# Kernel optimization log

Hardware: AMD Instinct MI355X
Metric: run time of the kernel (lower is better)

## Reference

```python
import jax, jax.numpy as jnp
import numpy as np

BIG = 1e9
EPS_BETA = 1e-6
EPS_BN = 1e-5

N_NODES = 50000
N_EDGES = 800000
IN_DIM = 128
OUT_DIM = 128


def setup_inputs() -> dict:
    key = jax.random.key(0)
    ks = jax.random.split(key, 8)
    h = jax.random.normal(ks[0], (N_NODES, IN_DIM), dtype=jnp.float32)
    src = jax.random.randint(ks[1], (N_EDGES,), 0, N_NODES, dtype=jnp.int32)
    dst = jax.random.randint(ks[2], (N_EDGES,), 0, N_NODES, dtype=jnp.int32)
    sigma_GD = jax.random.uniform(ks[3], (N_EDGES,), dtype=jnp.float32)
    fc_w = jax.random.normal(ks[4], (IN_DIM, OUT_DIM), dtype=jnp.float32) / np.sqrt(IN_DIM)
    fc_b = jax.random.normal(ks[5], (OUT_DIM,), dtype=jnp.float32) * 0.01
    attn_w = jax.random.normal(ks[6], (2 * OUT_DIM, 1), dtype=jnp.float32) / np.sqrt(2 * OUT_DIM)
    attn_b = jax.random.normal(ks[7], (1,), dtype=jnp.float32) * 0.01
    bn_gamma = jnp.ones((OUT_DIM,), dtype=jnp.float32)
    bn_beta = jnp.zeros((OUT_DIM,), dtype=jnp.float32)
    return {"h": h, "src": src, "dst": dst, "sigma_GD": sigma_GD,
            "fc_w": fc_w, "fc_b": fc_b, "attn_w": attn_w, "attn_b": attn_b,
            "bn_gamma": bn_gamma, "bn_beta": bn_beta}


def reference(h, src, dst, sigma_GD, fc_w, fc_b, attn_w, attn_b, bn_gamma, bn_beta):
    n = h.shape[0]
    # node projection
    z = h @ fc_w + fc_b                                   # [N, D]
    z = jnp.where(jnp.isinf(z), BIG, z)
    # per-edge attention logits: concat(src,dst) @ W == src@W1 + dst@W2 (avoid concat materialization)
    d = z.shape[1]
    w_src, w_dst = attn_w[:d], attn_w[d:]
    z_src = z[src]                                        # [E, D]
    a = z_src @ w_src + z[dst] @ w_dst + attn_b           # [E, 1]
    a = jnp.where(jnp.isinf(a), BIG, a)
    e = jax.nn.leaky_relu(a, negative_slope=0.01)[:, 0]   # [E]
    # segment softmax over incoming edges (mailbox softmax)
    m = jax.ops.segment_max(e, dst, num_segments=n)       # [N]
    ex = jnp.exp(e - m[dst])
    denom = jax.ops.segment_sum(ex, dst, num_segments=n)  # [N]
    alpha = ex / denom[dst]                               # [E]
    # beta: sigma_GD normalized per destination node
    bsum = jax.ops.segment_sum(sigma_GD, dst, num_segments=n)
    beta = sigma_GD / (bsum[dst] + EPS_BETA)              # [E]
    # weighted scatter-sum of source features
    h_new = jax.ops.segment_sum((alpha * beta)[:, None] * z_src, dst, num_segments=n)  # [N, D]
    h_new = jnp.where(jnp.isinf(h_new), BIG, h_new)
    # BatchNorm1d (training-mode batch stats, biased variance, as torch does)
    mu = h_new.mean(axis=0)
    var = ((h_new - mu) ** 2).mean(axis=0)
    h_bn = (h_new - mu) * jax.lax.rsqrt(var + EPS_BN) * bn_gamma + bn_beta
    return jax.nn.elu(h_bn)
```

## Files before the change

### kernel.cpp

```cpp
#include <hip/hip_runtime.h>
#include <hip/hip_fp16.h>
#include <math.h>

#define N_NODES 50000
#define N_EDGES 800000
#define BIGV 1000000000.0f
#define NBLK_GEMM 3125
#define CHUNK 4096
#define NBLK_A 196
#define NBUCKET 196

typedef _Float16 half8 __attribute__((ext_vector_type(8)));
typedef float floatx4 __attribute__((ext_vector_type(4)));

__device__ __forceinline__ float clampinf(float x) { return isinf(x) ? BIGV : x; }

__device__ __forceinline__ void barrier_lgkm_only() {
    __builtin_amdgcn_sched_barrier(0);
    asm volatile("s_waitcnt lgkmcnt(0)" ::: "memory");
    __builtin_amdgcn_s_barrier();
    __builtin_amdgcn_sched_barrier(0);
}

__global__ __launch_bounds__(256) void k_prep(const float* __restrict__ W,
                                              __half* __restrict__ wt,
                                              float* __restrict__ bns,
                                              const int* __restrict__ dst,
                                              int* __restrict__ counts)
{
    __shared__ int hist[NBUCKET];
    const int t = threadIdx.x;
    const int idx = blockIdx.x * 256 + t;
    if (idx < 16384) {
        int n = idx >> 7, k = idx & 127;
        wt[idx] = __float2half(W[k * 128 + n]);
    }
    if (idx < 256) bns[idx] = 0.f;
    if (t < NBUCKET) hist[t] = 0;
    __syncthreads();
    const int base = blockIdx.x * CHUNK;
    for (int i = t; i < CHUNK; i += 256) {
        int e = base + i;
        if (e < N_EDGES) atomicAdd(&hist[dst[e] >> 8], 1);
    }
    __syncthreads();
    if (t < NBUCKET) counts[blockIdx.x * NBUCKET + t] = hist[t];
}

__global__ __launch_bounds__(256) void k_gemm(
    const float* __restrict__ h, const __half* __restrict__ wt,
    const float* __restrict__ bias, const float* __restrict__ attn_w,
    __half* __restrict__ zh, float* __restrict__ sv, float* __restrict__ tv)
{
    __shared__ _Float16 hA[16][136];
    __shared__ float spart[4][16], tpart[4][16];

    const int tid = threadIdx.x;
    const int lane = tid & 63;
    const int wv = tid >> 6;
    const int l16 = lane & 15;
    const int oct = lane >> 4;
    const int n0 = wv << 5;
    const int node0 = blockIdx.x << 4;

    {
        const float4* h4 = (const float4*)(h + (size_t)node0 * 128);
        for (int i = tid; i < 512; i += 256) {
            int r = i >> 5, c4 = i & 31;
            float4 v = h4[i];
            union { __half2 h2[2]; uint2 u; } pk;
            pk.h2[0] = __floats2half2_rn(v.x, v.y);
            pk.h2[1] = __floats2half2_rn(v.z, v.w);
            *(uint2*)&hA[r][c4 << 2] = pk.u;
        }
    }

    half8 bfrag[4][2];
    #pragma unroll
    for (int kk = 0; kk < 4; ++kk)
        #pragma unroll
        for (int t = 0; t < 2; ++t)
            bfrag[kk][t] = *(const half8*)(wt + (size_t)(n0 + t * 16 + l16) * 128
                                              + kk * 32 + oct * 8);

    const float bv0 = bias[n0 + l16],         bv1 = bias[n0 + 16 + l16];
    const float ws0 = attn_w[n0 + l16],       ws1 = attn_w[n0 + 16 + l16];
    const float wd0 = attn_w[128 + n0 + l16], wd1 = attn_w[128 + n0 + 16 + l16];

    barrier_lgkm_only();

    floatx4 acc0 = {0.f, 0.f, 0.f, 0.f};
    floatx4 acc1 = {0.f, 0.f, 0.f, 0.f};
    #pragma unroll
    for (int kk = 0; kk < 4; ++kk) {
        half8 a = *(const half8*)&hA[l16][(kk << 5) + (oct << 3)];
        acc0 = __builtin_amdgcn_mfma_f32_16x16x32_f16(a, bfrag[kk][0], acc0, 0, 0, 0);
        acc1 = __builtin_amdgcn_mfma_f32_16x16x32_f16(a, bfrag[kk][1], acc1, 0, 0, 0);
    }

    float s_acc[4], t_acc[4];
    #pragma unroll
    for (int r = 0; r < 4; ++r) {
        float z0 = clampinf(acc0[r] + bv0);
        float z1 = clampinf(acc1[r] + bv1);
        const int row = (oct << 2) + r;
        zh[(size_t)(node0 + row) * 128 + n0 + l16]      = __float2half(z0);
        zh[(size_t)(node0 + row) * 128 + n0 + 16 + l16] = __float2half(z1);
        s_acc[r] = z0 * ws0 + z1 * ws1;
        t_acc[r] = z0 * wd0 + z1 * wd1;
    }
    #pragma unroll
    for (int r = 0; r < 4; ++r) {
        #pragma unroll
        for (int o = 1; o < 16; o <<= 1) {
            s_acc[r] += __shfl_xor(s_acc[r], o);
            t_acc[r] += __shfl_xor(t_acc[r], o);
        }
    }
    if (l16 == 0) {
        #pragma unroll
        for (int r = 0; r < 4; ++r) {
            spart[wv][(oct << 2) + r] = s_acc[r];
            tpart[wv][(oct << 2) + r] = t_acc[r];
        }
    }
    barrier_lgkm_only();
    if (tid < 16) {
        sv[node0 + tid] = spart[0][tid] + spart[1][tid] + spart[2][tid] + spart[3][tid];
        tv[node0 + tid] = tpart[0][tid] + tpart[1][tid] + tpart[2][tid] + tpart[3][tid];
    }
}

__global__ __launch_bounds__(256) void k_scatterA(const int* __restrict__ dst,
                                                  const int* __restrict__ counts,
                                                  int* __restrict__ tmp,
                                                  int* __restrict__ bbase_g)
{
    __shared__ int cur[NBUCKET];
    __shared__ int stot[256];
    const int t = threadIdx.x;
    const int self = blockIdx.x;
    int pre = 0, tot = 0;
    if (t < NBUCKET) {
        for (int b = 0; b < NBLK_A; ++b) {
            int c = counts[b * NBUCKET + t];
            if (b < self) pre += c;
            tot += c;
        }
    }
    stot[t] = (t < NBUCKET) ? tot : 0;
    __syncthreads();
    for (int off = 1; off < 256; off <<= 1) {
        int u = (t >= off) ? stot[t - off] : 0;
        __syncthreads();
        stot[t] += u;
        __syncthreads();
    }
    if (t < NBUCKET) {
        const int bb = stot[t] - tot;
        cur[t] = bb + pre;
        if (self == 0) bbase_g[t] = bb;
    }
    if (self == 0 && t == 0) bbase_g[NBUCKET] = N_EDGES;
    __syncthreads();
    const int base = self * CHUNK;
    for (int i = t; i < CHUNK; i += 256) {
        int e = base + i;
        if (e < N_EDGES) {
            int pos = atomicAdd(&cur[dst[e] >> 8], 1);
            tmp[pos] = e;
        }
    }
}

__global__ __launch_bounds__(256) void k_binB(
    const int* __restrict__ tmp, const int* __restrict__ bbase_g,
    const int* __restrict__ dst, const int* __restrict__ src,
    const float* __restrict__ sigma,
    const float* __restrict__ sv, const float* __restrict__ tv,
    const float* __restrict__ attn_b,
    int* __restrict__ colptr, float4* __restrict__ recs)
{
    __shared__ int hist[256];
    __shared__ int scn[256];
    __shared__ int cur[256];
    const int t = threadIdx.x;
    const int b = blockIdx.x;
    const int s0 = bbase_g[b];
    const int n = bbase_g[b + 1] - s0;
    hist[t] = 0;
    __syncthreads();
    for (int i = t; i < n; i += 256) {
        int e = tmp[s0 + i];
        atomicAdd(&hist[dst[e] & 255], 1);
    }
    __syncthreads();
    scn[t] = hist[t];
    __syncthreads();
    for (int off = 1; off < 256; off <<= 1) {
        int u = (t >= off) ? scn[t - off] : 0;
        __syncthreads();
        scn[t] += u;
        __syncthreads();
    }
    const int excl = scn[t] - hist[t];
    cur[t] = s0 + excl;
    const int node = (b << 8) + t;
    if (node < N_NODES) colptr[node] = s0 + excl;
    if (b == 0 && t == 0) colptr[N_NODES] = N_EDGES;
    __syncthreads();
    const float ab = attn_b[0];
    for (int i = t; i < n; i += 256) {
        int e = tmp[s0 + i];
        int d = dst[e];
        int pos = atomicAdd(&cur[d & 255], 1);
        int s = src[e];
        float a = sv[s] + tv[d] + ab;
        a = clampinf(a);
        float ev = a > 0.f ? a : 0.01f * a;
        float4 rec;
        rec.x = __int_as_float(s);
        rec.y = sigma[e];
        rec.z = ev;
        rec.w = 0.f;
        recs[pos] = rec;
    }
}

__global__ __launch_bounds__(256) void k_agg(
    const int* __restrict__ colptr, const float4* __restrict__ recs,
    const __half* __restrict__ zh, float* __restrict__ out)
{
    const int lane = threadIdx.x & 63;
    const int node = blockIdx.x * 4 + (threadIdx.x >> 6);
    if (node >= N_NODES) return;
    const int base = colptr[node];
    const int deg = colptr[node + 1] - base;

    const int grp = lane >> 4;
    const int l16 = lane & 15;
    float acc[8] = {0.f, 0.f, 0.f, 0.f, 0.f, 0.f, 0.f, 0.f};

    if (deg > 0) {
        if (deg <= 64) {
            int sidx = 0; float sig = 0.f, e = -INFINITY;
            if (lane < deg) {
                float4 r = recs[base + lane];
                sidx = __float_as_int(r.x); sig = r.y; e = r.z;
            }
            float m = e;
            for (int o = 32; o; o >>= 1) m = fmaxf(m, __shfl_xor(m, o));
            float p = (lane < deg) ? __expf(e - m) : 0.f;
            float dn = p, bs = sig;
            for (int o = 32; o; o >>= 1) {
                dn += __shfl_xor(dn, o);
                bs += __shfl_xor(bs, o);
            }
            const float coef = p * sig * (1.0f / dn) / (bs + 1e-6f);
            for (int c = 0; c < deg; c += 4) {
                const int j = c + grp;
                const int js = (j < deg) ? j : 0;
                float cf = __shfl(coef, js);
                int sj = __shfl(sidx, js);
                if (j < deg) {
                    uint4 raw = *(const uint4*)(zh + ((size_t)sj << 7) + (l16 << 3));
                    const __half2* hp = (const __half2*)&raw;
                    #pragma unroll
                    for (int k = 0; k < 4; ++k) {
                        float2 f = __half22float2(hp[k]);
                        acc[2*k]   = fmaf(cf, f.x, acc[2*k]);
                        acc[2*k+1] = fmaf(cf, f.y, acc[2*k+1]);
                    }
                }
            }
        } else {
            float m = -INFINITY;
            for (int i = lane; i < deg; i += 64) m = fmaxf(m, recs[base + i].z);
            for (int o = 32; o; o >>= 1) m = fmaxf(m, __shfl_xor(m, o));
            float dn = 0.f, bs = 0.f;
            for (int i = lane; i < deg; i += 64) {
                float4 r = recs[base + i];
                dn += __expf(r.z - m); bs += r.y;
            }
            for (int o = 32; o; o >>= 1) {
                dn += __shfl_xor(dn, o);
                bs += __shfl_xor(bs, o);
            }
            const float scale = (1.0f / dn) / (bs + 1e-6f);
            for (int c = 0; c < deg; c += 64) {
                int i = c + lane;
                int sidx = 0; float coef = 0.f;
                if (i < deg) {
                    float4 r = recs[base + i];
                    sidx = __float_as_int(r.x);
                    coef = __expf(r.z - m) * r.y * scale;
                }
                const int cnt2 = min(64, deg - c);
                for (int j = 0; j < cnt2; j += 4) {
                    const int jj = j + grp;
                    const int js = (jj < cnt2) ? jj : 0;
                    float cf = __shfl(coef, js);
                    int sj = __shfl(sidx, js);
                    if (jj < cnt2) {
                        uint4 raw = *(const uint4*)(zh + ((size_t)sj << 7) + (l16 << 3));
                        const __half2* hp = (const __half2*)&raw;
                        #pragma unroll
                        for (int k = 0; k < 4; ++k) {
                            float2 f = __half22float2(hp[k]);
                            acc[2*k]   = fmaf(cf, f.x, acc[2*k]);
                            acc[2*k+1] = fmaf(cf, f.y, acc[2*k+1]);
                        }
                    }
                }
            }
        }
    }
    #pragma unroll
    for (int k = 0; k < 8; ++k) {
        acc[k] += __shfl_xor(acc[k], 16);
        acc[k] += __shfl_xor(acc[k], 32);
    }
    if (grp == 0) {
        float4 o0, o1;
        o0.x = clampinf(acc[0]); o0.y = clampinf(acc[1]);
        o0.z = clampinf(acc[2]); o0.w = clampinf(acc[3]);
        o1.x = clampinf(acc[4]); o1.y = clampinf(acc[5]);
        o1.z = clampinf(acc[6]); o1.w = clampinf(acc[7]);
        float4* op = (float4*)(out + (size_t)node * 128 + (l16 << 3));
        op[0] = o0; op[1] = o1;
    }
}

__global__ __launch_bounds__(256) void k_bnstats(const float* __restrict__ hnew,
                                                 float* __restrict__ sums)
{
    const int tid = threadIdx.x;
    const int f4 = (tid & 31) << 2;
    const int rgrp = tid >> 5;
    float4 s = {0.f, 0.f, 0.f, 0.f}, q = {0.f, 0.f, 0.f, 0.f};
    for (int node = blockIdx.x * 8 + rgrp; node < N_NODES; node += 256 * 8) {
        float4 v = *(const float4*)(hnew + (size_t)node * 128 + f4);
        s.x += v.x; s.y += v.y; s.z += v.z; s.w += v.w;
        q.x += v.x * v.x; q.y += v.y * v.y; q.z += v.z * v.z; q.w += v.w * v.w;
    }
    __shared__ float4 ls[256], lq[256];
    ls[tid] = s; lq[tid] = q;
    __syncthreads();
    for (int off = 128; off >= 32; off >>= 1) {
        if (tid < off) {
            float4 a = ls[tid + off], b = lq[tid + off];
            ls[tid].x += a.x; ls[tid].y += a.y; ls[tid].z += a.z; ls[tid].w += a.w;
            lq[tid].x += b.x; lq[tid].y += b.y; lq[tid].z += b.z; lq[tid].w += b.w;
        }
        __syncthreads();
    }
    if (tid < 32) {
        float4 fs = ls[tid], fq = lq[tid];
        atomicAdd(&sums[f4 + 0], fs.x);
        atomicAdd(&sums[f4 + 1], fs.y);
        atomicAdd(&sums[f4 + 2], fs.z);
        atomicAdd(&sums[f4 + 3], fs.w);
        atomicAdd(&sums[128 + f4 + 0], fq.x);
        atomicAdd(&sums[128 + f4 + 1], fq.y);
        atomicAdd(&sums[128 + f4 + 2], fq.z);
        atomicAdd(&sums[128 + f4 + 3], fq.w);
    }
}

__global__ __launch_bounds__(256) void k_bnapply(float* __restrict__ io,
                                                 const float* __restrict__ sums,
                                                 const float* __restrict__ gamma,
                                                 const float* __restrict__ beta)
{
    __shared__ float sc[128], sh[128];
    const int tid = threadIdx.x;
    if (tid < 128) {
        const float invn = 1.0f / (float)N_NODES;
        float mu = sums[tid] * invn;
        float var = fmaxf(sums[128 + tid] * invn - mu * mu, 0.f);
        float g = gamma[tid] * rsqrtf(var + 1e-5f);
        sc[tid] = g;
        sh[tid] = beta[tid] - mu * g;
    }
    __syncthreads();
    const size_t idx = (size_t)blockIdx.x * 256 + tid;
    const int f4 = ((int)idx & 31) << 2;
    float4 x = ((const float4*)io)[idx];
    float y0 = x.x * sc[f4 + 0] + sh[f4 + 0];
    float y1 = x.y * sc[f4 + 1] + sh[f4 + 1];
    float y2 = x.z * sc[f4 + 2] + sh[f4 + 2];
    float y3 = x.w * sc[f4 + 3] + sh[f4 + 3];
    float4 o;
    o.x = y0 > 0.f ? y0 : expm1f(y0);
    o.y = y1 > 0.f ? y1 : expm1f(y1);
    o.z = y2 > 0.f ? y2 : expm1f(y2);
    o.w = y3 > 0.f ? y3 : expm1f(y3);
    ((float4*)io)[idx] = o;
}

extern "C" void kernel_launch(void* const* d_in, const int* in_sizes, int n_in,
                              void* d_out, int out_size, void* d_ws, size_t ws_size,
                              hipStream_t stream)
{
    const float* h      = (const float*)d_in[0];
    const int*   src    = (const int*)  d_in[1];
    const int*   dst    = (const int*)  d_in[2];
    const float* sigma  = (const float*)d_in[3];
    const float* fc_w   = (const float*)d_in[4];
    const float* fc_b   = (const float*)d_in[5];
    const float* attn_w = (const float*)d_in[6];
    const float* attn_b = (const float*)d_in[7];
    const float* gamma  = (const float*)d_in[8];
    const float* beta   = (const float*)d_in[9];
    float* out = (float*)d_out;

    float4* recs   = (float4*)d_ws;
    __half* zh     = (__half*)(recs + N_EDGES);
    float*  sv     = (float*)(zh + (size_t)N_NODES * 128);
    float*  tv     = sv + N_NODES;
    float*  bns    = tv + N_NODES;
    int*    colptr = (int*)(bns + 256);
    __half* wt     = (__half*)(colptr + 50004);
    int*    counts = (int*)(wt + 128 * 128);
    int*    bbase  = counts + 38416;
    int*    tmp    = bbase + 256;

    k_prep     <<<NBLK_A, 256, 0, stream>>>(fc_w, wt, bns, dst, counts);
    k_scatterA <<<NBLK_A, 256, 0, stream>>>(dst, counts, tmp, bbase);
    k_gemm     <<<NBLK_GEMM, 256, 0, stream>>>(h, wt, fc_b, attn_w, zh, sv, tv);
    k_binB     <<<NBUCKET, 256, 0, stream>>>(tmp, bbase, dst, src, sigma,
                                             sv, tv, attn_b, colptr, recs);
    k_agg      <<<N_NODES / 4, 256, 0, stream>>>(colptr, recs, zh, out);
    k_bnstats  <<<256, 256, 0, stream>>>(out, bns);
    k_bnapply  <<<(N_NODES * 128) / (256 * 4), 256, 0, stream>>>(out, bns, gamma, beta);
}
```

Measured before the change: 251.6 us.

## Move edge record building into bucket scatter and use finer 64-node buckets

The first-pass scatter now computes the attention logit and writes full float4 records, with dst packed in the last slot, into a bucket-sorted temp buffer. The second pass then only re-sorts records within 64-node buckets (782 buckets instead of 196), so there are no indirect re-reads of src/dst/sigma/sv/tv through the edge index. Finer buckets spread the second-pass sort over more blocks and let a wave shuffle replace the 256-entry shared-memory scan. In exchange the temp buffer grows from 4 to 16 bytes per edge, and the scatter kernel has to run after the GEMM, so it can no longer overlap with it.

```diff
diff --git a/kernel.cpp b/kernel.cpp
--- a/kernel.cpp
+++ b/kernel.cpp
@@ -7,8 +7,9 @@
 #define BIGV 1000000000.0f
 #define NBLK_GEMM 3125
 #define CHUNK 4096
-#define NBLK_A 196
-#define NBUCKET 196
+#define NCHUNK 196
+#define NBUCKET 782
+#define NB4 784
 
 typedef _Float16 half8 __attribute__((ext_vector_type(8)));
 typedef float floatx4 __attribute__((ext_vector_type(4)));
@@ -28,7 +29,7 @@
                                               const int* __restrict__ dst,
                                               int* __restrict__ counts)
 {
-    __shared__ int hist[NBUCKET];
+    __shared__ int hist[NB4];
     const int t = threadIdx.x;
     const int idx = blockIdx.x * 256 + t;
     if (idx < 16384) {
@@ -36,15 +37,15 @@
         wt[idx] = __float2half(W[k * 128 + n]);
     }
     if (idx < 256) bns[idx] = 0.f;
-    if (t < NBUCKET) hist[t] = 0;
+    for (int i = t; i < NB4; i += 256) hist[i] = 0;
     __syncthreads();
     const int base = blockIdx.x * CHUNK;
     for (int i = t; i < CHUNK; i += 256) {
         int e = base + i;
-        if (e < N_EDGES) atomicAdd(&hist[dst[e] >> 8], 1);
-    }
-    __syncthreads();
-    if (t < NBUCKET) counts[blockIdx.x * NBUCKET + t] = hist[t];
+        if (e < N_EDGES) atomicAdd(&hist[dst[e] >> 6], 1);
+    }
+    __syncthreads();
+    for (int i = t; i < NB4; i += 256) counts[blockIdx.x * NB4 + i] = hist[i];
 }
 
 __global__ __launch_bounds__(256) void k_gemm(
@@ -131,97 +132,112 @@
     }
 }
 
-__global__ __launch_bounds__(256) void k_scatterA(const int* __restrict__ dst,
-                                                  const int* __restrict__ counts,
-                                                  int* __restrict__ tmp,
-                                                  int* __restrict__ bbase_g)
-{
-    __shared__ int cur[NBUCKET];
-    __shared__ int stot[256];
+__global__ __launch_bounds__(256) void k_scat(
+    const int* __restrict__ src, const int* __restrict__ dst,
+    const float* __restrict__ sigma,
+    const float* __restrict__ sv, const float* __restrict__ tv,
+    const float* __restrict__ attn_b, const int* __restrict__ counts,
+    float4* __restrict__ tmp, int* __restrict__ bbase_g)
+{
+    __shared__ int cur[NB4];
+    __shared__ int tsc[256];
     const int t = threadIdx.x;
     const int self = blockIdx.x;
-    int pre = 0, tot = 0;
-    if (t < NBUCKET) {
-        for (int b = 0; b < NBLK_A; ++b) {
-            int c = counts[b * NBUCKET + t];
-            if (b < self) pre += c;
-            tot += c;
-        }
-    }
-    stot[t] = (t < NBUCKET) ? tot : 0;
+
+    uint4 pre = {0u, 0u, 0u, 0u}, tot = {0u, 0u, 0u, 0u};
+    if (t < 196) {
+        const uint4* c4 = (const uint4*)counts;
+        for (int c = 0; c < NCHUNK; ++c) {
+            uint4 v = c4[c * (NB4 / 4) + t];
+            tot.x += v.x; tot.y += v.y; tot.z += v.z; tot.w += v.w;
+            if (c < self) { pre.x += v.x; pre.y += v.y; pre.z += v.z; pre.w += v.w; }
+        }
+    }
+    const int tsum = (t < 196) ? (int)(tot.x + tot.y + tot.z + tot.w) : 0;
+    tsc[t] = tsum;
     __syncthreads();
     for (int off = 1; off < 256; off <<= 1) {
-        int u = (t >= off) ? stot[t - off] : 0;
+        int u = (t >= off) ? tsc[t - off] : 0;
         __syncthreads();
-        stot[t] += u;
+        tsc[t] += u;
         __syncthreads();
     }
-    if (t < NBUCKET) {
-        const int bb = stot[t] - tot;
-        cur[t] = bb + pre;
-        if (self == 0) bbase_g[t] = bb;
+    if (t < 196) {
+        const int v0 = tsc[t] - tsum;
+        const int v1 = v0 + (int)tot.x;
+        const int v2 = v1 + (int)tot.y;
+        const int v3 = v2 + (int)tot.z;
+        cur[4*t+0] = v0 + (int)pre.x;
+        cur[4*t+1] = v1 + (int)pre.y;
+        cur[4*t+2] = v2 + (int)pre.z;
+        cur[4*t+3] = v3 + (int)pre.w;
+        if (self == 0) {
+            bbase_g[4*t+0] = v0; bbase_g[4*t+1] = v1;
+            bbase_g[4*t+2] = v2; bbase_g[4*t+3] = v3;
+        }
     }
     if (self == 0 && t == 0) bbase_g[NBUCKET] = N_EDGES;
     __syncthreads();
+
+    const float ab = attn_b[0];
     const int base = self * CHUNK;
     for (int i = t; i < CHUNK; i += 256) {
         int e = base + i;
         if (e < N_EDGES) {
-            int pos = atomicAdd(&cur[dst[e] >> 8], 1);
-            tmp[pos] = e;
-        }
-    }
-}
-
-__global__ __launch_bounds__(256) void k_binB(
-    const int* __restrict__ tmp, const int* __restrict__ bbase_g,
-    const int* __restrict__ dst, const int* __restrict__ src,
-    const float* __restrict__ sigma,
-    const float* __restrict__ sv, const float* __restrict__ tv,
-    const float* __restrict__ attn_b,
-    int* __restrict__ colptr, float4* __restrict__ recs)
-{
-    __shared__ int hist[256];
-    __shared__ int scn[256];
-    __shared__ int cur[256];
+            int s = src[e];
+            int d = dst[e];
+            float a = sv[s] + tv[d] + ab;
+            a = clampinf(a);
+            float ev = a > 0.f ? a : 0.01f * a;
+            int pos = atomicAdd(&cur[d >> 6], 1);
+            float4 rec;
+            rec.x = __int_as_float(s);
+            rec.y = sigma[e];
+            rec.z = ev;
+            rec.w = __int_as_float(d);
+            tmp[pos] = rec;
+        }
+    }
+}
+
+__global__ __launch_bounds__(256) void k_binB(const float4* __restrict__ tmp,
+                                              const int* __restrict__ bbase_g,
+                                              int* __restrict__ colptr,
+                                              float4* __restrict__ recs)
+{
+    __shared__ int hist[64];
+    __shared__ int cur[64];
     const int t = threadIdx.x;
     const int b = blockIdx.x;
     const int s0 = bbase_g[b];
     const int n = bbase_g[b + 1] - s0;
-    hist[t] = 0;
-    __syncthreads();
+    if (t < 64) hist[t] = 0;
+    __syncthreads();
+    const float* tw = (const float*)tmp;
     for (int i = t; i < n; i += 256) {
-        int e = tmp[s0 + i];
-        atomicAdd(&hist[dst[e] & 255], 1);
-    }
-    __syncthreads();
-    scn[t] = hist[t];
-    __syncthreads();
-    for (int off = 1; off < 256; off <<= 1) {
-        int u = (t >= off) ? scn[t - off] : 0;
-        __syncthreads();
-        scn[t] += u;
-        __syncthreads();
-    }
-    const int excl = scn[t] - hist[t];
-    cur[t] = s0 + excl;
-    const int node = (b << 8) + t;
-    if (node < N_NODES) colptr[node] = s0 + excl;
+        int d = __float_as_int(tw[4 * (size_t)(s0 + i) + 3]);
+        atomicAdd(&hist[d & 63], 1);
+    }
+    __syncthreads();
+    if (t < 64) {
+        const int hv = hist[t];
+        int x = hv;
+        #pragma unroll
+        for (int o = 1; o < 64; o <<= 1) {
+            int u = __shfl_up(x, o);
+            if (t >= o) x += u;
+        }
+        const int excl = x - hv;
+        cur[t] = s0 + excl;
+        const int node = (b << 6) + t;
+        if (node < N_NODES) colptr[node] = s0 + excl;
+    }
     if (b == 0 && t == 0) colptr[N_NODES] = N_EDGES;
     __syncthreads();
-    const float ab = attn_b[0];
     for (int i = t; i < n; i += 256) {
-        int e = tmp[s0 + i];
-        int d = dst[e];
-        int pos = atomicAdd(&cur[d & 255], 1);
-        int s = src[e];
-        float a = sv[s] + tv[d] + ab;
-        a = clampinf(a);
-        float ev = a > 0.f ? a : 0.01f * a;
-        float4 rec;
-        rec.x = __int_as_float(s);
-        rec.y = sigma[e];
-        rec.z = ev;
+        float4 rec = tmp[s0 + i];
+        int d = __float_as_int(rec.w);
+        int pos = atomicAdd(&cur[d & 63], 1);
         rec.w = 0.f;
         recs[pos] = rec;
     }
@@ -415,22 +431,22 @@
     float* out = (float*)d_out;
 
     float4* recs   = (float4*)d_ws;
-    __half* zh     = (__half*)(recs + N_EDGES);
+    float4* tmp    = recs + N_EDGES;
+    __half* zh     = (__half*)(tmp + N_EDGES);
     float*  sv     = (float*)(zh + (size_t)N_NODES * 128);
     float*  tv     = sv + N_NODES;
     float*  bns    = tv + N_NODES;
     int*    colptr = (int*)(bns + 256);
     __half* wt     = (__half*)(colptr + 50004);
-    int*    counts = (int*)(wt + 128 * 128);
-    int*    bbase  = counts + 38416;
-    int*    tmp    = bbase + 256;
-
-    k_prep     <<<NBLK_A, 256, 0, stream>>>(fc_w, wt, bns, dst, counts);
-    k_scatterA <<<NBLK_A, 256, 0, stream>>>(dst, counts, tmp, bbase);
-    k_gemm     <<<NBLK_GEMM, 256, 0, stream>>>(h, wt, fc_b, attn_w, zh, sv, tv);
-    k_binB     <<<NBUCKET, 256, 0, stream>>>(tmp, bbase, dst, src, sigma,
-                                             sv, tv, attn_b, colptr, recs);
-    k_agg      <<<N_NODES / 4, 256, 0, stream>>>(colptr, recs, zh, out);
-    k_bnstats  <<<256, 256, 0, stream>>>(out, bns);
-    k_bnapply  <<<(N_NODES * 128) / (256 * 4), 256, 0, stream>>>(out, bns, gamma, beta);
-}
+    int*    counts = (int*)(wt + 16384);
+    int*    bbase  = counts + NCHUNK * NB4;
+
+    k_prep    <<<NCHUNK, 256, 0, stream>>>(fc_w, wt, bns, dst, counts);
+    k_gemm    <<<NBLK_GEMM, 256, 0, stream>>>(h, wt, fc_b, attn_w, zh, sv, tv);
+    k_scat    <<<NCHUNK, 256, 0, stream>>>(src, dst, sigma, sv, tv, attn_b,
+                                           counts, tmp, bbase);
+    k_binB    <<<NBUCKET, 256, 0, stream>>>(tmp, bbase, colptr, recs);
+    k_agg     <<<N_NODES / 4, 256, 0, stream>>>(colptr, recs, zh, out);
+    k_bnstats <<<256, 256, 0, stream>>>(out, bns);
+    k_bnapply <<<(N_NODES * 128) / (256 * 4), 256, 0, stream>>>(out, bns, gamma, beta);
+}
```

Result: faster. 235.5 us (-6.4%).
